# Kernel optimization log

Measured on AMD Instinct MI355X. Metric: run time of the kernel, lower is better.

Reference implementation:

```python
import jax, jax.numpy as jnp
import numpy as np

B, T, C = 4, 2048, 1024
H = 16
D = C // H  # 64


def setup_inputs() -> dict:
    key = jax.random.key(0)
    k1, k2, k3 = jax.random.split(key, 3)
    x = jax.random.normal(k1, (B, T, C), dtype=jnp.float32)
    W_attn = jax.random.normal(k2, (C, 3 * C), dtype=jnp.float32) * (1.0 / np.sqrt(C))
    W_proj = jax.random.normal(k3, (C, C), dtype=jnp.float32) * (1.0 / np.sqrt(C))
    return {"x": x, "W_attn": W_attn, "W_proj": W_proj}


def reference(x, W_attn, W_proj):
    b, t, c = x.shape
    # qkv projection: [B,T,3C]
    qkv = jnp.einsum('btc,cd->btd', x, W_attn)
    q, k, v = jnp.split(qkv, 3, axis=-1)
    # split heads -> [B,H,T,D]
    q = q.reshape(b, t, H, D).transpose(0, 2, 1, 3)
    k = k.reshape(b, t, H, D).transpose(0, 2, 1, 3)
    v = v.reshape(b, t, H, D).transpose(0, 2, 1, 3)
    # scores scaled by 1/sqrt(C) (faithful to source: uses full embed dim)
    att = jnp.einsum('bhtd,bhsd->bhts', q, k) * (1.0 / jnp.sqrt(jnp.float32(c)))
    # causal mask: -inf where key index > query index
    causal = jnp.tril(jnp.ones((t, t), dtype=bool))
    att = jnp.where(causal, att, jnp.float32(-jnp.inf))
    att = jax.nn.softmax(att, axis=-1)
    # attention output -> combine heads
    y = jnp.einsum('bhts,bhsd->bhtd', att, v)
    y = y.transpose(0, 2, 1, 3).reshape(b, t, c)
    z = jnp.einsum('btc,cd->btd', y, W_proj)
    return z
```

## Files before the change

kernel.cpp:

```cpp
#include <hip/hip_runtime.h>
#include <hip/hip_bf16.h>

typedef __bf16 bf16x8 __attribute__((ext_vector_type(8)));
typedef float f32x4 __attribute__((ext_vector_type(4)));

static __device__ __forceinline__ __bf16 tobf(float x) {
    __hip_bfloat16 h = __float2bfloat16(x);
    __bf16 r;
    __builtin_memcpy(&r, &h, 2);
    return r;
}

static __device__ __forceinline__ float fexp2(float x) {
    float r;
    asm("v_exp_f32 %0, %1" : "=v"(r) : "v"(x));
    return r;
}

__global__ __launch_bounds__(256) void prep_k(const float* __restrict__ x,
                                              __hip_bfloat16* __restrict__ x_bf,
                                              const float* __restrict__ Wa,
                                              __hip_bfloat16* __restrict__ WaT,
                                              const float* __restrict__ Wp,
                                              __hip_bfloat16* __restrict__ WpT) {
    __shared__ float tile[32][33];
    const int bid = blockIdx.x;
    const int tid = threadIdx.x;
    if (bid < 8192) {
        int i = bid * 256 + tid;
        float4 v = reinterpret_cast<const float4*>(x)[i];
        __hip_bfloat16 a = __float2bfloat16(v.x);
        __hip_bfloat16 b = __float2bfloat16(v.y);
        __hip_bfloat16 c = __float2bfloat16(v.z);
        __hip_bfloat16 d = __float2bfloat16(v.w);
        ushort4 o;
        o.x = *reinterpret_cast<unsigned short*>(&a);
        o.y = *reinterpret_cast<unsigned short*>(&b);
        o.z = *reinterpret_cast<unsigned short*>(&c);
        o.w = *reinterpret_cast<unsigned short*>(&d);
        reinterpret_cast<ushort4*>(x_bf)[i] = o;
        return;
    }
    const float* in;
    __hip_bfloat16* out;
    int bx, Cn, qrows;
    float qscale;
    int t;
    if (bid < 8192 + 3072) {
        t = bid - 8192;
        in = Wa; out = WaT; Cn = 3072; qrows = 1024;
        qscale = 0.045084223f;
        bx = t % 96;
    } else {
        t = bid - 11264;
        in = Wp; out = WpT; Cn = 1024; qrows = 0;
        qscale = 1.0f;
        bx = t % 32;
    }
    const int by = (bid < 11264) ? (t / 96) : (t / 32);
    const int R = 1024;
    const int c0 = bx * 32, r0 = by * 32;
    const int tx = tid & 31, ty = tid >> 5;
#pragma unroll
    for (int i = 0; i < 4; ++i)
        tile[ty + i * 8][tx] = in[(size_t)(r0 + ty + i * 8) * Cn + c0 + tx];
    __syncthreads();
#pragma unroll
    for (int i = 0; i < 4; ++i) {
        int orow = c0 + ty + i * 8;
        float v = tile[tx][ty + i * 8];
        if (orow < qrows) v *= qscale;
        out[(size_t)orow * R + r0 + tx] = __float2bfloat16(v);
    }
}

__global__ __launch_bounds__(256) void vtrans_k(const __hip_bfloat16* __restrict__ qkv,
                                                __hip_bfloat16* __restrict__ Vt) {
    __shared__ __attribute__((aligned(16))) __hip_bfloat16 lds[64 * 72];
    const int tt = blockIdx.x;
    const int bh = blockIdx.y;
    const int b = bh >> 4, h = bh & 15;
    const int tid = threadIdx.x;
    const __hip_bfloat16* src =
        qkv + (size_t)b * 2048 * 3072 + 2048 + h * 64 + (size_t)tt * 64 * 3072;
#pragma unroll
    for (int p = 0; p < 2; ++p) {
        int u = p * 256 + tid;
        int t_in = u >> 3, dc = u & 7;
        bf16x8 v = *reinterpret_cast<const bf16x8*>(src + (size_t)t_in * 3072 + dc * 8);
        *reinterpret_cast<bf16x8*>(&lds[t_in * 72 + dc * 8]) = v;
    }
    __syncthreads();
    __hip_bfloat16* dst = Vt + (size_t)bh * 64 * 2048 + tt * 64;
#pragma unroll
    for (int p = 0; p < 2; ++p) {
        int w = p * 256 + tid;
        int d = w >> 3, oc = w & 7;
        bf16x8 o;
#pragma unroll
        for (int e = 0; e < 8; ++e) {
            int s = oc * 8 + e;
            int r = (s & 3) | (((s >> 3) & 3) << 2) | (((s >> 2) & 1) << 4);
            int t_in = (s & 32) | r;
            o[e] = lds[t_in * 72 + d];
        }
        *reinterpret_cast<bf16x8*>(&dst[(size_t)d * 2048 + oc * 8]) = o;
    }
}

template <bool OUT_BF16>
__global__ __launch_bounds__(512, 4) void gemm8w(const __hip_bfloat16* __restrict__ A,
                                                 const __hip_bfloat16* __restrict__ Bt,
                                                 __hip_bfloat16* __restrict__ Cb,
                                                 float* __restrict__ Cf,
                                                 int M, int N, int K) {
    __shared__ __attribute__((aligned(16))) char As[2][64 * 128];
    __shared__ __attribute__((aligned(16))) char Bs[2][128 * 128];
    const int tid = threadIdx.x;
    const int lane = tid & 63, wid = tid >> 6;
    const int l15 = lane & 15, lg = lane >> 4;
    const int wr = wid >> 2, wc = wid & 3;
    const int lin = blockIdx.y * gridDim.x + blockIdx.x;
    const int cpx = (gridDim.x * gridDim.y) >> 3;
    const int sw = (lin & 7) * cpx + (lin >> 3);
    const int bn = sw % gridDim.x, bm = sw / gridDim.x;
    const size_t arow0 = (size_t)bm * 128;
    const size_t brow0 = (size_t)bn * 256;

    f32x4 acc[4][4] = {};

    const int arp = tid >> 3, apu = (tid & 7) ^ (arp & 7);
    const int aR = 2 * arp + (apu >> 2), aC = (apu & 3) * 8;
    const int b1i = 512 + tid;
    const int brp1 = b1i >> 3, bpu1 = (b1i & 7) ^ (brp1 & 7);
    const int bR1 = 2 * brp1 + (bpu1 >> 2), bC1 = (bpu1 & 3) * 8;

    const __hip_bfloat16* pa = A + (arow0 + aR) * (size_t)K + aC;
    const __hip_bfloat16* pb0 = Bt + (brow0 + aR) * (size_t)K + aC;
    const __hip_bfloat16* pb1 = Bt + (brow0 + bR1) * (size_t)K + bC1;

    auto stage = [&](int buf) {
        char* Ad = &As[buf][0];
        char* Bd = &Bs[buf][0];
        __builtin_amdgcn_global_load_lds(
            (const __attribute__((address_space(1))) void*)pa,
            (__attribute__((address_space(3))) void*)(Ad + tid * 16), 16, 0, 0);
        __builtin_amdgcn_global_load_lds(
            (const __attribute__((address_space(1))) void*)pb0,
            (__attribute__((address_space(3))) void*)(Bd + tid * 16), 16, 0, 0);
        __builtin_amdgcn_global_load_lds(
            (const __attribute__((address_space(1))) void*)pb1,
            (__attribute__((address_space(3))) void*)(Bd + (512 + tid) * 16), 16, 0, 0);
        pa += 32;
        pb0 += 32;
        pb1 += 32;
    };

    stage(0);
    asm volatile("s_waitcnt vmcnt(0)" ::: "memory");
    __syncthreads();

    const int nk = K >> 5;
    int cur = 0;
    for (int kt = 0; kt < nk; ++kt) {
        if (kt + 1 < nk) stage(cur ^ 1);
        const char* Ab = cur ? &As[1][0] : &As[0][0];
        const char* Bb = cur ? &Bs[1][0] : &Bs[0][0];
        bf16x8 af[4], bfr[4];
#pragma unroll
        for (int mf = 0; mf < 4; ++mf) {
            int R = wr * 64 + mf * 16 + l15;
            int rp = R >> 1;
            int p = (((R & 1) << 2) + lg) ^ (rp & 7);
            af[mf] = *reinterpret_cast<const bf16x8*>(Ab + rp * 128 + p * 16);
        }
#pragma unroll
        for (int nf = 0; nf < 4; ++nf) {
            int R = wc * 64 + nf * 16 + l15;
            int rp = R >> 1;
            int p = (((R & 1) << 2) + lg) ^ (rp & 7);
            bfr[nf] = *reinterpret_cast<const bf16x8*>(Bb + rp * 128 + p * 16);
        }
        __builtin_amdgcn_s_setprio(1);
#pragma unroll
        for (int mf = 0; mf < 4; ++mf)
#pragma unroll
            for (int nf = 0; nf < 4; ++nf)
                acc[mf][nf] = __builtin_amdgcn_mfma_f32_16x16x32_bf16(af[mf], bfr[nf],
                                                                      acc[mf][nf], 0, 0, 0);
        __builtin_amdgcn_s_setprio(0);
        asm volatile("s_waitcnt vmcnt(0)" ::: "memory");
        __syncthreads();
        cur ^= 1;
    }

#pragma unroll
    for (int mf = 0; mf < 4; ++mf) {
#pragma unroll
        for (int nf = 0; nf < 4; ++nf) {
#pragma unroll
            for (int j = 0; j < 4; ++j) {
                int row = bm * 128 + wr * 64 + mf * 16 + lg * 4 + j;
                int col = bn * 256 + wc * 64 + nf * 16 + l15;
                if (OUT_BF16)
                    Cb[(size_t)row * N + col] = __float2bfloat16(acc[mf][nf][j]);
                else
                    Cf[(size_t)row * N + col] = acc[mf][nf][j];
            }
        }
    }
}

__global__ __launch_bounds__(256) void attn_k(const __hip_bfloat16* __restrict__ qkv,
                                              const __hip_bfloat16* __restrict__ Vt,
                                              __hip_bfloat16* __restrict__ y) {
    constexpr int TT = 2048;
    constexpr int S3C = 3072;
    const int bh = blockIdx.x, b = bh >> 4, h = bh & 15;
    const int st = 15 - (int)blockIdx.y;
    const int tid = threadIdx.x;
    const int wid = tid >> 6, lane = tid & 63;
    const int l15 = lane & 15, lg = lane >> 4;

    __shared__ __attribute__((aligned(16))) char Ks[2][64 * 128];
    __shared__ __attribute__((aligned(16))) char Vs[2][64 * 128];

    const __hip_bfloat16* base = qkv + (size_t)b * TT * S3C;
    const int qo = h * 64, ko = 1024 + h * 64;
    const __hip_bfloat16* vt = Vt + (size_t)bh * 64 * TT;

    bf16x8 vones;
#pragma unroll
    for (int i = 0; i < 8; ++i) vones[i] = tobf(1.0f);

    const int idx0 = tid, idx1 = 256 + tid;
    const int r0 = idx0 >> 3, c0 = 8 * ((idx0 & 7) ^ (r0 & 7));
    const int r1 = idx1 >> 3, c1 = 8 * ((idx1 & 7) ^ (r1 & 7));

    const int qbase = st * 128 + wid * 32;
    const int my_nt = (qbase >> 6) + 1;
    const int blk_nt = st * 2 + 2;

    bf16x8 aq[2][2];
#pragma unroll
    for (int m = 0; m < 2; ++m) {
        const __hip_bfloat16* qp = base + (size_t)(qbase + m * 16 + l15) * S3C + qo + lg * 8;
        aq[m][0] = *reinterpret_cast<const bf16x8*>(qp);
        aq[m][1] = *reinterpret_cast<const bf16x8*>(qp + 32);
    }

    f32x4 acc[2][4] = {};
    f32x4 lsum[2] = {};

    const __hip_bfloat16* kp0 = base + (size_t)r0 * S3C + ko + c0;
    const __hip_bfloat16* kp1 = base + (size_t)r1 * S3C + ko + c1;
    const __hip_bfloat16* vp0 = vt + (size_t)r0 * TT + c0;
    const __hip_bfloat16* vp1 = vt + (size_t)r1 * TT + c1;

    auto stage = [&](int buf) {
        char* Kd = buf ? &Ks[1][0] : &Ks[0][0];
        char* Vd = buf ? &Vs[1][0] : &Vs[0][0];
        __builtin_amdgcn_global_load_lds(
            (const __attribute__((address_space(1))) void*)kp0,
            (__attribute__((address_space(3))) void*)(Kd + idx0 * 16), 16, 0, 0);
        __builtin_amdgcn_global_load_lds(
            (const __attribute__((address_space(1))) void*)kp1,
            (__attribute__((address_space(3))) void*)(Kd + idx1 * 16), 16, 0, 0);
        __builtin_amdgcn_global_load_lds(
            (const __attribute__((address_space(1))) void*)vp0,
            (__attribute__((address_space(3))) void*)(Vd + idx0 * 16), 16, 0, 0);
        __builtin_amdgcn_global_load_lds(
            (const __attribute__((address_space(1))) void*)vp1,
            (__attribute__((address_space(3))) void*)(Vd + idx1 * 16), 16, 0, 0);
        kp0 += (size_t)64 * S3C;
        kp1 += (size_t)64 * S3C;
        vp0 += 64;
        vp1 += 64;
    };

    stage(0);
    asm volatile("s_waitcnt vmcnt(0)" ::: "memory");
    __syncthreads();

    int cur = 0;
    for (int kt = 0; kt < blk_nt; ++kt) {
        if (kt + 1 < blk_nt) stage(cur ^ 1);
        if (kt < my_nt) {
            const int kb = kt * 64;
            const char* Kb = cur ? &Ks[1][0] : &Ks[0][0];
            const char* Vb = cur ? &Vs[1][0] : &Vs[0][0];
            const int swl = l15 & 7;
            f32x4 s[2][4];
            __builtin_amdgcn_s_setprio(1);
#pragma unroll
            for (int cg = 0; cg < 4; ++cg) {
                const char* krow = Kb + (cg * 16 + l15) * 128;
                bf16x8 k0 = *reinterpret_cast<const bf16x8*>(krow + 16 * (lg ^ swl));
                bf16x8 k1 = *reinterpret_cast<const bf16x8*>(krow + 16 * ((4 + lg) ^ swl));
#pragma unroll
                for (int m = 0; m < 2; ++m) {
                    f32x4 z = {0.f, 0.f, 0.f, 0.f};
                    z = __builtin_amdgcn_mfma_f32_16x16x32_bf16(k0, aq[m][0], z, 0, 0, 0);
                    z = __builtin_amdgcn_mfma_f32_16x16x32_bf16(k1, aq[m][1], z, 0, 0, 0);
                    s[m][cg] = z;
                }
            }
            __builtin_amdgcn_s_setprio(0);
            bf16x8 vb[2][4];
#pragma unroll
            for (int dg = 0; dg < 4; ++dg) {
                const char* vrow = Vb + (dg * 16 + l15) * 128;
                vb[0][dg] = *reinterpret_cast<const bf16x8*>(vrow + 16 * (lg ^ swl));
                vb[1][dg] = *reinterpret_cast<const bf16x8*>(vrow + 16 * ((4 + lg) ^ swl));
            }
            float p[2][4][4];
            const bool needmask = (kb + 63 > qbase);
#pragma unroll
            for (int m = 0; m < 2; ++m)
#pragma unroll
                for (int cg = 0; cg < 4; ++cg)
#pragma unroll
                    for (int j = 0; j < 4; ++j) {
                        float e = fexp2(s[m][cg][j]);
                        if (needmask) {
                            int key = kb + cg * 16 + lg * 4 + j;
                            int qrow = qbase + m * 16 + l15;
                            e = (key > qrow) ? 0.f : e;
                        }
                        p[m][cg][j] = e;
                    }
            bf16x8 pa[2][2];
#pragma unroll
            for (int m = 0; m < 2; ++m)
#pragma unroll
                for (int ks = 0; ks < 2; ++ks) {
                    bf16x8 tt2;
                    tt2[0] = tobf(p[m][2 * ks][0]);
                    tt2[1] = tobf(p[m][2 * ks][1]);
                    tt2[2] = tobf(p[m][2 * ks][2]);
                    tt2[3] = tobf(p[m][2 * ks][3]);
                    tt2[4] = tobf(p[m][2 * ks + 1][0]);
                    tt2[5] = tobf(p[m][2 * ks + 1][1]);
                    tt2[6] = tobf(p[m][2 * ks + 1][2]);
                    tt2[7] = tobf(p[m][2 * ks + 1][3]);
                    pa[m][ks] = tt2;
                }
            __builtin_amdgcn_s_setprio(1);
#pragma unroll
            for (int ks = 0; ks < 2; ++ks) {
#pragma unroll
                for (int dg = 0; dg < 4; ++dg)
#pragma unroll
                    for (int m = 0; m < 2; ++m)
                        acc[m][dg] = __builtin_amdgcn_mfma_f32_16x16x32_bf16(
                            pa[m][ks], vb[ks][dg], acc[m][dg], 0, 0, 0);
#pragma unroll
                for (int m = 0; m < 2; ++m)
                    lsum[m] = __builtin_amdgcn_mfma_f32_16x16x32_bf16(pa[m][ks], vones,
                                                                      lsum[m], 0, 0, 0);
            }
            __builtin_amdgcn_s_setprio(0);
        }
        asm volatile("s_waitcnt vmcnt(0)" ::: "memory");
        __syncthreads();
        cur ^= 1;
    }

#pragma unroll
    for (int m = 0; m < 2; ++m)
#pragma unroll
        for (int j = 0; j < 4; ++j) {
            float inv = 1.f / lsum[m][j];
            int t = qbase + m * 16 + lg * 4 + j;
#pragma unroll
            for (int dg = 0; dg < 4; ++dg) {
                float o = acc[m][dg][j] * inv;
                y[((size_t)(b * TT + t)) * 1024 + h * 64 + dg * 16 + l15] = __float2bfloat16(o);
            }
        }
}

extern "C" void kernel_launch(void* const* d_in, const int* in_sizes, int n_in,
                              void* d_out, int out_size, void* d_ws, size_t ws_size,
                              hipStream_t stream) {
    const float* x = (const float*)d_in[0];
    const float* Wa = (const float*)d_in[1];
    const float* Wp = (const float*)d_in[2];
    float* out = (float*)d_out;

    __hip_bfloat16* ws = (__hip_bfloat16*)d_ws;
    __hip_bfloat16* x_bf = ws;
    __hip_bfloat16* WaT = x_bf + (size_t)8192 * 1024;
    __hip_bfloat16* WpT = WaT + (size_t)3072 * 1024;
    __hip_bfloat16* qkv = WpT + (size_t)1024 * 1024;
    __hip_bfloat16* ybf = qkv + (size_t)8192 * 3072;
    __hip_bfloat16* Vt = ybf + (size_t)8192 * 1024;

    prep_k<<<8192 + 3072 + 1024, 256, 0, stream>>>(x, x_bf, Wa, WaT, Wp, WpT);
    gemm8w<true><<<dim3(12, 64), 512, 0, stream>>>(x_bf, WaT, qkv, nullptr, 8192, 3072, 1024);
    vtrans_k<<<dim3(32, 64), 256, 0, stream>>>(qkv, Vt);
    attn_k<<<dim3(64, 16), 256, 0, stream>>>(qkv, Vt, ybf);
    gemm8w<false><<<dim3(4, 64), 512, 0, stream>>>(ybf, WpT, nullptr, out, 8192, 1024, 1024);
}
```

Baseline: 171.8 us.

## Switch GEMMs to 4-wave 128x128 tiles with BK=64 and row-swizzled LDS

Replaces the 8-wave 128x256 GEMM (K-step 32) with a 4-wave 128x128 tile kernel that stages 64-wide K slices. The LDS layout changes to a per-row XOR swizzle. Each wave does two MFMA sub-steps per barrier, which halves the number of barriers and gives more blocks in the grid. The trade-off is less operand reuse per block and more LDS per block, which may lower occupancy.

```diff
diff --git a/kernel.cpp b/kernel.cpp
--- a/kernel.cpp
+++ b/kernel.cpp
@@ -109,86 +109,87 @@
 }
 
 template <bool OUT_BF16>
-__global__ __launch_bounds__(512, 4) void gemm8w(const __hip_bfloat16* __restrict__ A,
+__global__ __launch_bounds__(256, 2) void gemm4w(const __hip_bfloat16* __restrict__ A,
                                                  const __hip_bfloat16* __restrict__ Bt,
                                                  __hip_bfloat16* __restrict__ Cb,
                                                  float* __restrict__ Cf,
                                                  int M, int N, int K) {
-    __shared__ __attribute__((aligned(16))) char As[2][64 * 128];
+    __shared__ __attribute__((aligned(16))) char As[2][128 * 128];
     __shared__ __attribute__((aligned(16))) char Bs[2][128 * 128];
     const int tid = threadIdx.x;
     const int lane = tid & 63, wid = tid >> 6;
     const int l15 = lane & 15, lg = lane >> 4;
-    const int wr = wid >> 2, wc = wid & 3;
+    const int wr = wid >> 1, wc = wid & 1;
     const int lin = blockIdx.y * gridDim.x + blockIdx.x;
     const int cpx = (gridDim.x * gridDim.y) >> 3;
     const int sw = (lin & 7) * cpx + (lin >> 3);
     const int bn = sw % gridDim.x, bm = sw / gridDim.x;
     const size_t arow0 = (size_t)bm * 128;
-    const size_t brow0 = (size_t)bn * 256;
+    const size_t brow0 = (size_t)bn * 128;
 
     f32x4 acc[4][4] = {};
 
-    const int arp = tid >> 3, apu = (tid & 7) ^ (arp & 7);
-    const int aR = 2 * arp + (apu >> 2), aC = (apu & 3) * 8;
-    const int b1i = 512 + tid;
-    const int brp1 = b1i >> 3, bpu1 = (b1i & 7) ^ (brp1 & 7);
-    const int bR1 = 2 * brp1 + (bpu1 >> 2), bC1 = (bpu1 & 3) * 8;
-
-    const __hip_bfloat16* pa = A + (arow0 + aR) * (size_t)K + aC;
-    const __hip_bfloat16* pb0 = Bt + (brow0 + aR) * (size_t)K + aC;
-    const __hip_bfloat16* pb1 = Bt + (brow0 + bR1) * (size_t)K + bC1;
+    const __hip_bfloat16* pa[4];
+    const __hip_bfloat16* pb[4];
+#pragma unroll
+    for (int p = 0; p < 4; ++p) {
+        int idx = p * 256 + tid;
+        int row = idx >> 3, c = idx & 7;
+        int col = 8 * (c ^ (row & 7));
+        pa[p] = A + (arow0 + row) * (size_t)K + col;
+        pb[p] = Bt + (brow0 + row) * (size_t)K + col;
+    }
 
     auto stage = [&](int buf) {
-        char* Ad = &As[buf][0];
-        char* Bd = &Bs[buf][0];
-        __builtin_amdgcn_global_load_lds(
-            (const __attribute__((address_space(1))) void*)pa,
-            (__attribute__((address_space(3))) void*)(Ad + tid * 16), 16, 0, 0);
-        __builtin_amdgcn_global_load_lds(
-            (const __attribute__((address_space(1))) void*)pb0,
-            (__attribute__((address_space(3))) void*)(Bd + tid * 16), 16, 0, 0);
-        __builtin_amdgcn_global_load_lds(
-            (const __attribute__((address_space(1))) void*)pb1,
-            (__attribute__((address_space(3))) void*)(Bd + (512 + tid) * 16), 16, 0, 0);
-        pa += 32;
-        pb0 += 32;
-        pb1 += 32;
+        char* Ad = buf ? &As[1][0] : &As[0][0];
+        char* Bd = buf ? &Bs[1][0] : &Bs[0][0];
+#pragma unroll
+        for (int p = 0; p < 4; ++p) {
+            __builtin_amdgcn_global_load_lds(
+                (const __attribute__((address_space(1))) void*)pa[p],
+                (__attribute__((address_space(3))) void*)(Ad + (p * 256 + tid) * 16), 16, 0, 0);
+            __builtin_amdgcn_global_load_lds(
+                (const __attribute__((address_space(1))) void*)pb[p],
+                (__attribute__((address_space(3))) void*)(Bd + (p * 256 + tid) * 16), 16, 0, 0);
+            pa[p] += 64;
+            pb[p] += 64;
+        }
     };
 
     stage(0);
     asm volatile("s_waitcnt vmcnt(0)" ::: "memory");
     __syncthreads();
 
-    const int nk = K >> 5;
+    const int nk = K >> 6;
     int cur = 0;
     for (int kt = 0; kt < nk; ++kt) {
         if (kt + 1 < nk) stage(cur ^ 1);
         const char* Ab = cur ? &As[1][0] : &As[0][0];
         const char* Bb = cur ? &Bs[1][0] : &Bs[0][0];
-        bf16x8 af[4], bfr[4];
-#pragma unroll
-        for (int mf = 0; mf < 4; ++mf) {
-            int R = wr * 64 + mf * 16 + l15;
-            int rp = R >> 1;
-            int p = (((R & 1) << 2) + lg) ^ (rp & 7);
-            af[mf] = *reinterpret_cast<const bf16x8*>(Ab + rp * 128 + p * 16);
-        }
-#pragma unroll
-        for (int nf = 0; nf < 4; ++nf) {
-            int R = wc * 64 + nf * 16 + l15;
-            int rp = R >> 1;
-            int p = (((R & 1) << 2) + lg) ^ (rp & 7);
-            bfr[nf] = *reinterpret_cast<const bf16x8*>(Bb + rp * 128 + p * 16);
-        }
-        __builtin_amdgcn_s_setprio(1);
-#pragma unroll
-        for (int mf = 0; mf < 4; ++mf)
-#pragma unroll
-            for (int nf = 0; nf < 4; ++nf)
-                acc[mf][nf] = __builtin_amdgcn_mfma_f32_16x16x32_bf16(af[mf], bfr[nf],
-                                                                      acc[mf][nf], 0, 0, 0);
-        __builtin_amdgcn_s_setprio(0);
+#pragma unroll
+        for (int ks = 0; ks < 2; ++ks) {
+            bf16x8 af[4], bfr[4];
+#pragma unroll
+            for (int mf = 0; mf < 4; ++mf) {
+                int R = wr * 64 + mf * 16 + l15;
+                af[mf] = *reinterpret_cast<const bf16x8*>(
+                    Ab + R * 128 + 16 * ((ks * 4 + lg) ^ (R & 7)));
+            }
+#pragma unroll
+            for (int nf = 0; nf < 4; ++nf) {
+                int R = wc * 64 + nf * 16 + l15;
+                bfr[nf] = *reinterpret_cast<const bf16x8*>(
+                    Bb + R * 128 + 16 * ((ks * 4 + lg) ^ (R & 7)));
+            }
+            __builtin_amdgcn_s_setprio(1);
+#pragma unroll
+            for (int mf = 0; mf < 4; ++mf)
+#pragma unroll
+                for (int nf = 0; nf < 4; ++nf)
+                    acc[mf][nf] = __builtin_amdgcn_mfma_f32_16x16x32_bf16(af[mf], bfr[nf],
+                                                                          acc[mf][nf], 0, 0, 0);
+            __builtin_amdgcn_s_setprio(0);
+        }
         asm volatile("s_waitcnt vmcnt(0)" ::: "memory");
         __syncthreads();
         cur ^= 1;
@@ -201,7 +202,7 @@
 #pragma unroll
             for (int j = 0; j < 4; ++j) {
                 int row = bm * 128 + wr * 64 + mf * 16 + lg * 4 + j;
-                int col = bn * 256 + wc * 64 + nf * 16 + l15;
+                int col = bn * 128 + wc * 64 + nf * 16 + l15;
                 if (OUT_BF16)
                     Cb[(size_t)row * N + col] = __float2bfloat16(acc[mf][nf][j]);
                 else
@@ -397,8 +398,8 @@
     __hip_bfloat16* Vt = ybf + (size_t)8192 * 1024;
 
     prep_k<<<8192 + 3072 + 1024, 256, 0, stream>>>(x, x_bf, Wa, WaT, Wp, WpT);
-    gemm8w<true><<<dim3(12, 64), 512, 0, stream>>>(x_bf, WaT, qkv, nullptr, 8192, 3072, 1024);
+    gemm4w<true><<<dim3(24, 64), 256, 0, stream>>>(x_bf, WaT, qkv, nullptr, 8192, 3072, 1024);
     vtrans_k<<<dim3(32, 64), 256, 0, stream>>>(qkv, Vt);
     attn_k<<<dim3(64, 16), 256, 0, stream>>>(qkv, Vt, ybf);
-    gemm8w<false><<<dim3(4, 64), 512, 0, stream>>>(ybf, WpT, nullptr, out, 8192, 1024, 1024);
-}
+    gemm4w<false><<<dim3(8, 64), 256, 0, stream>>>(ybf, WpT, nullptr, out, 8192, 1024, 1024);
+}
```

Measured after the change: 165.6 us. 1.04x faster.
